# Performance work log

Hardware: AMD Instinct MI355X
Metric: run time of the kernel (lower is better)

Reference implementation:

```python
import jax, jax.numpy as jnp
import numpy as np

B, S, HID = 4096, 50, 256
NH = 4
HD = HID // NH          # 64
FB = S // 2 + 1         # 26 freq bins
ALPHA = 0.3
LN_EPS = 1e-12


def setup_inputs() -> dict:
    key = jax.random.key(0)
    ks = jax.random.split(key, 10)
    item = jax.random.normal(ks[0], (B, S, HID), dtype=jnp.float32)
    attr = jax.random.normal(ks[1], (B, S, HID), dtype=jnp.float32)
    complex_weight = jax.random.normal(ks[2], (1, NH, S // 2, HD), dtype=jnp.float32) * 0.02
    base_filter = jnp.ones((NH, FB, 1), dtype=jnp.float32)
    base_bias = jnp.full((NH, FB, 1), -0.1, dtype=jnp.float32)
    # adaptive MLP: Linear(HID,HID) -> GELU -> Linear(HID, NH*FB*2)
    w1 = jax.random.normal(ks[3], (HID, HID), dtype=jnp.float32) * (1.0 / np.sqrt(HID))
    b1 = jnp.zeros((HID,), dtype=jnp.float32)
    w2 = jax.random.normal(ks[4], (HID, NH * FB * 2), dtype=jnp.float32) * (1.0 / np.sqrt(HID))
    b2 = jnp.zeros((NH * FB * 2,), dtype=jnp.float32)
    ln_gamma = jnp.ones((HID,), dtype=jnp.float32)
    ln_beta = jnp.zeros((HID,), dtype=jnp.float32)
    return {
        "item_tensor": item, "attr_tensor": attr,
        "complex_weight": complex_weight,
        "base_filter": base_filter, "base_bias": base_bias,
        "w1": w1, "b1": b1, "w2": w2, "b2": b2,
        "ln_gamma": ln_gamma, "ln_beta": ln_beta,
    }


def _forward(item_tensor, attr_tensor, complex_weight, base_filter, base_bias,
             w1, b1, w2, b2, ln_gamma, ln_beta):
    b, s, hid = item_tensor.shape
    # [B, NH, S, HD]
    x_heads = item_tensor.reshape(b, s, NH, HD).transpose(0, 2, 1, 3)

    # ---- frequency branch ----
    F_fft = jnp.fft.rfft(x_heads, axis=2, norm='ortho')  # [B, NH, FB, HD] complex
    attr_ctx = attr_tensor.mean(axis=1)                   # [B, HID]
    h = jax.nn.gelu(attr_ctx @ w1 + b1, approximate=False)
    adapt = (h @ w2 + b2).reshape(b, NH, FB, 2)
    adaptive_scale = adapt[..., 0:1]
    adaptive_bias = adapt[..., 1:2]
    eff_filter = base_filter * (1.0 + adaptive_scale)     # [B, NH, FB, 1]
    eff_bias = base_bias + adaptive_bias                   # real, added to real part
    F_mod = F_fft * eff_filter + eff_bias
    x_fft = jnp.fft.irfft(F_mod, n=s, axis=2, norm='ortho')  # [B, NH, S, HD]

    # ---- Haar wavelet lifting branch (S even => no truncation/pad) ----
    x_even = x_heads[:, :, 0::2, :]
    x_odd = x_heads[:, :, 1::2, :]
    approx = 0.5 * (x_even + x_odd)
    detail = 0.5 * (x_even - x_odd) * complex_weight
    even_recon = approx + detail
    odd_recon = approx - detail
    # interleave even/odd back: [B, NH, S/2, 2, HD] -> [B, NH, S, HD]
    x_wavelet = jnp.stack([even_recon, odd_recon], axis=3).reshape(b, NH, s, HD)

    # ---- gate combine + residual LayerNorm ----
    x_combined = (1.0 - ALPHA) * x_wavelet + ALPHA * x_fft
    x_out = x_combined.transpose(0, 2, 1, 3).reshape(b, s, hid)
    res = x_out + item_tensor  # dropout is identity in eval
    mu = res.mean(axis=-1, keepdims=True)
    var = jnp.mean(jnp.square(res - mu), axis=-1, keepdims=True)
    return (res - mu) * jax.lax.rsqrt(var + LN_EPS) * ln_gamma + ln_beta


def reference(item_tensor, attr_tensor, complex_weight, base_filter, base_bias,
              w1, b1, w2, b2, ln_gamma, ln_beta):
    return _forward(item_tensor, attr_tensor, complex_weight, base_filter, base_bias,
                    w1, b1, w2, b2, ln_gamma, ln_beta)
```

## Files before the change

kernel.cpp:

```cpp
#include <hip/hip_runtime.h>
#include <math.h>
#include <utility>

#define B_    4096
#define S_    50
#define HID_  256
#define NH_   4
#define HD_   64
#define FB_   26
#define NPAIR 25
#define CHUNK 10

__device__ __forceinline__ float rfl_f(float v) {
    union { float f; int i; } u;
    u.f = v;
    u.i = __builtin_amdgcn_readfirstlane(u.i);
    return u.f;
}

__global__ void precompute_kernel(const float* __restrict__ base_filter,
                                  const float* __restrict__ base_bias,
                                  const float* __restrict__ w2,
                                  const float* __restrict__ b2,
                                  float* __restrict__ Wp,
                                  float* __restrict__ C0)
{
    const int m   = blockIdx.x;
    const int j   = threadIdx.x;
    const int h   = m / 100;
    const int rem = m % 100;
    const int cls = rem / 50;
    const int tau = rem % 50;

    const float inv50  = 1.0f / 50.0f;
    const float invs50 = 0.141421356237309515f;

    float acc   = 0.0f;
    float c0acc = 0.0f;
    for (int k = 0; k < FB_; ++k) {
        int   mm   = (k * tau) % 50;
        float cosv = cospif((float)(2 * mm) / 50.0f);
        float wk   = (k == 0 || k == 25) ? 1.0f : 2.0f;
        int   o    = (h * FB_ + k) * 2 + cls;
        float coef;
        if (cls == 0) coef = wk * inv50 * cosv * base_filter[h * FB_ + k];
        else          coef = wk * invs50 * cosv;
        acc += coef * w2[j * 208 + o];
        if (j == 0) {
            if (cls == 0) c0acc += coef * (1.0f + b2[o]);
            else          c0acc += coef * (base_bias[h * FB_ + k] + b2[o]);
        }
    }
    Wp[j * 400 + m] = acc;
    if (j == 0) C0[m] = c0acc;
}

__global__ __launch_bounds__(256)
void mean_kernel(const float* __restrict__ attr, float* __restrict__ ctx)
{
    const int g    = threadIdx.x >> 6;
    const int lane = threadIdx.x & 63;
    const int b    = blockIdx.x * 4 + g;
    const float4* p = (const float4*)(attr + (size_t)b * S_ * HID_) + lane;
    float4 s = make_float4(0.f, 0.f, 0.f, 0.f);
    #pragma unroll
    for (int t = 0; t < S_; ++t) {
        float4 v = p[t * 64];
        s.x += v.x; s.y += v.y; s.z += v.z; s.w += v.w;
    }
    const float is = 1.0f / S_;
    s.x *= is; s.y *= is; s.z *= is; s.w *= is;
    ((float4*)(ctx + (size_t)b * HID_))[lane] = s;
}

template <int EPI>
__global__ __launch_bounds__(256)
void gemm_kernel(const float* __restrict__ A, const float* __restrict__ Bm,
                 const float* __restrict__ bias, float* __restrict__ C,
                 int M, int N, int K)
{
    __shared__ float As[64][33];
    __shared__ float Bs[32][64];
    const int tid = threadIdx.x;
    const int tx = tid & 15, ty = tid >> 4;
    const int col0 = blockIdx.x * 64;
    const int row0 = blockIdx.y * 64;

    float acc[4][4] = {};

    for (int k0 = 0; k0 < K; k0 += 32) {
        #pragma unroll
        for (int l = 0; l < 2; ++l) {
            int f = tid + l * 256;
            int r = f >> 3;
            int c4 = f & 7;
            float4 av = *(const float4*)(A + (size_t)(row0 + r) * K + k0 + c4 * 4);
            As[r][c4 * 4 + 0] = av.x; As[r][c4 * 4 + 1] = av.y;
            As[r][c4 * 4 + 2] = av.z; As[r][c4 * 4 + 3] = av.w;
        }
        #pragma unroll
        for (int l = 0; l < 2; ++l) {
            int f = tid + l * 256;
            int kr = f >> 4;
            int c4 = f & 15;
            int col = col0 + c4 * 4;
            float4 bv = make_float4(0.f, 0.f, 0.f, 0.f);
            if (col < N) bv = *(const float4*)(Bm + (size_t)(k0 + kr) * N + col);
            *(float4*)&Bs[kr][c4 * 4] = bv;
        }
        __syncthreads();
        #pragma unroll
        for (int kk = 0; kk < 32; ++kk) {
            float4 bv = *(float4*)&Bs[kk][tx * 4];
            float br[4] = {bv.x, bv.y, bv.z, bv.w};
            #pragma unroll
            for (int r = 0; r < 4; ++r) {
                float av = As[ty * 4 + r][kk];
                #pragma unroll
                for (int c = 0; c < 4; ++c)
                    acc[r][c] = fmaf(av, br[c], acc[r][c]);
            }
        }
        __syncthreads();
    }

    #pragma unroll
    for (int r = 0; r < 4; ++r) {
        int row = row0 + ty * 4 + r;
        #pragma unroll
        for (int c = 0; c < 4; ++c) {
            int col = col0 + tx * 4 + c;
            if (col < N) {
                float v = acc[r][c] + bias[col];
                if (EPI == 0)
                    v = 0.5f * v * (1.0f + erff(v * 0.70710678118654752f));
                C[(size_t)row * N + col] = v;
            }
        }
    }
}

template <int T, int TP>
__device__ __forceinline__ float cval(const float (&cv)[26]) {
    constexpr int ci = ((T - TP) % 50 + 50) % 50;
    constexpr int dd = (ci > 25) ? (50 - ci) : ci;
    return cv[dd];
}

template <int R0, int TP, int... J>
__device__ __forceinline__ void convJ(float (&a)[CHUNK], const float (&x)[50],
                                      const float (&cv)[26],
                                      std::integer_sequence<int, J...>) {
    ((a[J] = fmaf(cval<R0 + J, TP>(cv), x[TP], a[J])), ...);
}

template <int R0, int... TPs>
__device__ __forceinline__ void convChunk(float (&a)[CHUNK], const float (&x)[50],
                                          const float (&cv)[26],
                                          std::integer_sequence<int, TPs...>) {
    (convJ<R0, TPs>(a, x, cv, std::make_integer_sequence<int, CHUNK>{}), ...);
}

template <int R0>
__device__ __forceinline__ void chunk_proc(const float (&x)[50], const float (&cv)[26],
                                           const float* __restrict__ vb,
                                           const float* __restrict__ cwp,
                                           float gam, float bet,
                                           float* __restrict__ outp,
                                           float (*buf)[HID_], float2* sums,
                                           int tid, int w, int lane)
{
    float a[CHUNK] = {};
    convChunk<R0>(a, x, cv, std::make_integer_sequence<int, 50>{});

    #pragma unroll
    for (int q = 0; q < CHUNK / 2; ++q) {
        const int p = R0 / 2 + q;
        float e  = x[2 * p], o = x[2 * p + 1];
        float ap = 0.5f * (e + o);
        float dt = 0.5f * (e - o) * cwp[p * HD_];
        float fe = a[2 * q]     + rfl_f(vb[2 * p]);
        float fo = a[2 * q + 1] + rfl_f(vb[2 * p + 1]);
        a[2 * q]     = 0.7f * (ap + dt) + 0.3f * fe + e;
        a[2 * q + 1] = 0.7f * (ap - dt) + 0.3f * fo + o;
    }

    #pragma unroll
    for (int j = 0; j < CHUNK; ++j) buf[j][tid] = a[j];
    __syncthreads();

    #pragma unroll
    for (int rr = 0; rr < 3; ++rr) {
        const int r = w + rr * 4;
        if (r < CHUNK) {
            float4 v = *(const float4*)&buf[r][lane * 4];
            float s  = (v.x + v.y) + (v.z + v.w);
            float qq = v.x * v.x + v.y * v.y + v.z * v.z + v.w * v.w;
            #pragma unroll
            for (int m = 1; m < 64; m <<= 1) {
                s  += __shfl_xor(s,  m, 64);
                qq += __shfl_xor(qq, m, 64);
            }
            if (lane == 0) {
                float mu  = s * (1.0f / HID_);
                float var = qq * (1.0f / HID_) - mu * mu;
                sums[r] = make_float2(mu, rsqrtf(var + 1e-12f));
            }
        }
    }
    __syncthreads();

    #pragma unroll
    for (int j = 0; j < CHUNK; ++j) {
        float2 ms = sums[j];
        outp[(R0 + j) * HID_] = (a[j] - ms.x) * ms.y * gam + bet;
    }
}

__global__ __launch_bounds__(256)
__attribute__((amdgpu_waves_per_eu(2)))
void fused_kernel(const float* __restrict__ item,
                  const float* __restrict__ cw,
                  const float* __restrict__ cv,
                  const float* __restrict__ gamma,
                  const float* __restrict__ beta,
                  float* __restrict__ out)
{
    __shared__ float  buf[CHUNK][HID_];
    __shared__ float2 sums[CHUNK];

    const int b    = blockIdx.x;
    const int tid  = threadIdx.x;
    const int w    = tid >> 6;
    const int lane = tid & 63;
    const int wu   = __builtin_amdgcn_readfirstlane(w);

    const float* cb = cv + (size_t)b * 400 + wu * 100;
    float cvr[26];
    #pragma unroll
    for (int j = 0; j < 26; ++j)
        cvr[j] = rfl_f(cb[j]);
    const float* vb = cb + 50;

    const float* xp = item + (size_t)b * S_ * HID_ + tid;
    float x[50];
    #pragma unroll
    for (int t = 0; t < 50; ++t) x[t] = xp[t * HID_];

    const float gam = gamma[tid];
    const float bet = beta[tid];
    float* outp = out + (size_t)b * S_ * HID_ + tid;
    const float* cwp = cw + (size_t)(wu * NPAIR) * HD_ + lane;

    chunk_proc< 0>(x, cvr, vb, cwp, gam, bet, outp, buf, sums, tid, w, lane);
    chunk_proc<10>(x, cvr, vb, cwp, gam, bet, outp, buf, sums, tid, w, lane);
    chunk_proc<20>(x, cvr, vb, cwp, gam, bet, outp, buf, sums, tid, w, lane);
    chunk_proc<30>(x, cvr, vb, cwp, gam, bet, outp, buf, sums, tid, w, lane);
    chunk_proc<40>(x, cvr, vb, cwp, gam, bet, outp, buf, sums, tid, w, lane);
}

extern "C" void kernel_launch(void* const* d_in, const int* in_sizes, int n_in,
                              void* d_out, int out_size, void* d_ws, size_t ws_size,
                              hipStream_t stream)
{
    (void)in_sizes; (void)n_in; (void)out_size; (void)ws_size;
    const float* item = (const float*)d_in[0];
    const float* attr = (const float*)d_in[1];
    const float* cw   = (const float*)d_in[2];
    const float* bf   = (const float*)d_in[3];
    const float* bb   = (const float*)d_in[4];
    const float* w1   = (const float*)d_in[5];
    const float* b1   = (const float*)d_in[6];
    const float* w2   = (const float*)d_in[7];
    const float* b2   = (const float*)d_in[8];
    const float* g    = (const float*)d_in[9];
    const float* be   = (const float*)d_in[10];
    float* out = (float*)d_out;
    float* ws  = (float*)d_ws;

    float* ctx  = ws;
    float* hbuf = ws + 1048576;
    float* Wp   = ws + 2097152;
    float* C0   = ws + 2199552;
    float* cvb  = ws + 2200064;

    hipLaunchKernelGGL(precompute_kernel, dim3(400), dim3(256), 0, stream,
                       bf, bb, w2, b2, Wp, C0);
    hipLaunchKernelGGL(mean_kernel, dim3(B_ / 4), dim3(256), 0, stream, attr, ctx);
    hipLaunchKernelGGL((gemm_kernel<0>), dim3(4, 64), dim3(256), 0, stream,
                       ctx, w1, b1, hbuf, B_, 256, 256);
    hipLaunchKernelGGL((gemm_kernel<1>), dim3(7, 64), dim3(256), 0, stream,
                       hbuf, Wp, C0, cvb, B_, 400, 256);
    hipLaunchKernelGGL(fused_kernel, dim3(B_), dim3(256), 0, stream,
                       item, cw, cvb, g, be, out);
}
```

Baseline: 590.6 us.

## Stream item pairs into 50-row register accumulators and fold gate/residual constants

The fused kernel no longer holds all 50 input rows in registers and convolves them in chunks. It now streams item rows two at a time into 50 register accumulators that start from the per-row bias. The 0.3 gate is folded into the precomputed filter coefficients, and the wavelet, gate and residual terms are merged into two FMA coefficients per pair. Occupancy is raised from 2 to 4 waves per EU, and both small GEMMs switch to 32x32 tiles to launch more blocks. The aims are fewer registers, better overlap of loads with FMAs and better GEMM occupancy, at the risk of spills with 50 live accumulators under a tighter register cap.

```diff
diff --git a/kernel.cpp b/kernel.cpp
--- a/kernel.cpp
+++ b/kernel.cpp
@@ -9,7 +9,6 @@
 #define HD_   64
 #define FB_   26
 #define NPAIR 25
-#define CHUNK 10
 
 __device__ __forceinline__ float rfl_f(float v) {
     union { float f; int i; } u;
@@ -32,8 +31,8 @@
     const int cls = rem / 50;
     const int tau = rem % 50;
 
-    const float inv50  = 1.0f / 50.0f;
-    const float invs50 = 0.141421356237309515f;
+    const float inv50  = 0.3f / 50.0f;
+    const float invs50 = 0.3f * 0.141421356237309515f;
 
     float acc   = 0.0f;
     float c0acc = 0.0f;
@@ -79,57 +78,43 @@
                  const float* __restrict__ bias, float* __restrict__ C,
                  int M, int N, int K)
 {
-    __shared__ float As[64][33];
-    __shared__ float Bs[32][64];
+    __shared__ float As[32][36];
+    __shared__ float Bs[32][36];
     const int tid = threadIdx.x;
     const int tx = tid & 15, ty = tid >> 4;
-    const int col0 = blockIdx.x * 64;
-    const int row0 = blockIdx.y * 64;
-
-    float acc[4][4] = {};
+    const int col0 = blockIdx.x * 32;
+    const int row0 = blockIdx.y * 32;
+    const int lr = tid >> 3;
+    const int lc = (tid & 7) * 4;
+
+    float acc[2][2] = {};
 
     for (int k0 = 0; k0 < K; k0 += 32) {
-        #pragma unroll
-        for (int l = 0; l < 2; ++l) {
-            int f = tid + l * 256;
-            int r = f >> 3;
-            int c4 = f & 7;
-            float4 av = *(const float4*)(A + (size_t)(row0 + r) * K + k0 + c4 * 4);
-            As[r][c4 * 4 + 0] = av.x; As[r][c4 * 4 + 1] = av.y;
-            As[r][c4 * 4 + 2] = av.z; As[r][c4 * 4 + 3] = av.w;
-        }
-        #pragma unroll
-        for (int l = 0; l < 2; ++l) {
-            int f = tid + l * 256;
-            int kr = f >> 4;
-            int c4 = f & 15;
-            int col = col0 + c4 * 4;
-            float4 bv = make_float4(0.f, 0.f, 0.f, 0.f);
-            if (col < N) bv = *(const float4*)(Bm + (size_t)(k0 + kr) * N + col);
-            *(float4*)&Bs[kr][c4 * 4] = bv;
-        }
+        float4 av = *(const float4*)(A + (size_t)(row0 + lr) * K + k0 + lc);
+        *(float4*)&As[lr][lc] = av;
+        float4 bv = make_float4(0.f, 0.f, 0.f, 0.f);
+        if (col0 + lc + 4 <= N)
+            bv = *(const float4*)(Bm + (size_t)(k0 + lr) * N + col0 + lc);
+        *(float4*)&Bs[lr][lc] = bv;
         __syncthreads();
         #pragma unroll
         for (int kk = 0; kk < 32; ++kk) {
-            float4 bv = *(float4*)&Bs[kk][tx * 4];
-            float br[4] = {bv.x, bv.y, bv.z, bv.w};
-            #pragma unroll
-            for (int r = 0; r < 4; ++r) {
-                float av = As[ty * 4 + r][kk];
-                #pragma unroll
-                for (int c = 0; c < 4; ++c)
-                    acc[r][c] = fmaf(av, br[c], acc[r][c]);
-            }
+            float a0 = As[ty * 2][kk],     a1 = As[ty * 2 + 1][kk];
+            float b0 = Bs[kk][tx * 2],     b1 = Bs[kk][tx * 2 + 1];
+            acc[0][0] = fmaf(a0, b0, acc[0][0]);
+            acc[0][1] = fmaf(a0, b1, acc[0][1]);
+            acc[1][0] = fmaf(a1, b0, acc[1][0]);
+            acc[1][1] = fmaf(a1, b1, acc[1][1]);
         }
         __syncthreads();
     }
 
     #pragma unroll
-    for (int r = 0; r < 4; ++r) {
-        int row = row0 + ty * 4 + r;
+    for (int r = 0; r < 2; ++r) {
+        int row = row0 + ty * 2 + r;
         #pragma unroll
-        for (int c = 0; c < 4; ++c) {
-            int col = col0 + tx * 4 + c;
+        for (int c = 0; c < 2; ++c) {
+            int col = col0 + tx * 2 + c;
             if (col < N) {
                 float v = acc[r][c] + bias[col];
                 if (EPI == 0)
@@ -147,52 +132,54 @@
     return cv[dd];
 }
 
-template <int R0, int TP, int... J>
-__device__ __forceinline__ void convJ(float (&a)[CHUNK], const float (&x)[50],
-                                      const float (&cv)[26],
-                                      std::integer_sequence<int, J...>) {
-    ((a[J] = fmaf(cval<R0 + J, TP>(cv), x[TP], a[J])), ...);
-}
-
-template <int R0, int... TPs>
-__device__ __forceinline__ void convChunk(float (&a)[CHUNK], const float (&x)[50],
+template <int P, int... T>
+__device__ __forceinline__ void convPairT(float (&acc)[50], float e, float o,
                                           const float (&cv)[26],
-                                          std::integer_sequence<int, TPs...>) {
-    (convJ<R0, TPs>(a, x, cv, std::make_integer_sequence<int, CHUNK>{}), ...);
+                                          std::integer_sequence<int, T...>) {
+    ((acc[T] = fmaf(cval<T, 2 * P>(cv), e, acc[T])), ...);
+    ((acc[T] = fmaf(cval<T, 2 * P + 1>(cv), o, acc[T])), ...);
+}
+
+template <int P>
+__device__ __forceinline__ void convPair(float (&acc)[50],
+                                         const float* __restrict__ xp,
+                                         const float* __restrict__ cwp,
+                                         const float (&cv)[26]) {
+    float e   = xp[(2 * P) * HID_];
+    float o   = xp[(2 * P + 1) * HID_];
+    float cwv = cwp[P * HD_];
+    convPairT<P>(acc, e, o, cv, std::make_integer_sequence<int, 50>{});
+    float Pc = fmaf(0.35f, cwv, 1.35f);
+    float Qc = fmaf(-0.35f, cwv, 0.35f);
+    acc[2 * P]     = fmaf(Pc, e, acc[2 * P]);
+    acc[2 * P]     = fmaf(Qc, o, acc[2 * P]);
+    acc[2 * P + 1] = fmaf(Qc, e, acc[2 * P + 1]);
+    acc[2 * P + 1] = fmaf(Pc, o, acc[2 * P + 1]);
+}
+
+template <int... Ps>
+__device__ __forceinline__ void convAll(float (&acc)[50],
+                                        const float* __restrict__ xp,
+                                        const float* __restrict__ cwp,
+                                        const float (&cv)[26],
+                                        std::integer_sequence<int, Ps...>) {
+    (convPair<Ps>(acc, xp, cwp, cv), ...);
 }
 
 template <int R0>
-__device__ __forceinline__ void chunk_proc(const float (&x)[50], const float (&cv)[26],
-                                           const float* __restrict__ vb,
-                                           const float* __restrict__ cwp,
-                                           float gam, float bet,
-                                           float* __restrict__ outp,
-                                           float (*buf)[HID_], float2* sums,
-                                           int tid, int w, int lane)
-{
-    float a[CHUNK] = {};
-    convChunk<R0>(a, x, cv, std::make_integer_sequence<int, 50>{});
-
-    #pragma unroll
-    for (int q = 0; q < CHUNK / 2; ++q) {
-        const int p = R0 / 2 + q;
-        float e  = x[2 * p], o = x[2 * p + 1];
-        float ap = 0.5f * (e + o);
-        float dt = 0.5f * (e - o) * cwp[p * HD_];
-        float fe = a[2 * q]     + rfl_f(vb[2 * p]);
-        float fo = a[2 * q + 1] + rfl_f(vb[2 * p + 1]);
-        a[2 * q]     = 0.7f * (ap + dt) + 0.3f * fe + e;
-        a[2 * q + 1] = 0.7f * (ap - dt) + 0.3f * fo + o;
-    }
-
-    #pragma unroll
-    for (int j = 0; j < CHUNK; ++j) buf[j][tid] = a[j];
+__device__ __forceinline__ void lnChunk(float (&acc)[50], float (*buf)[HID_],
+                                        float2* sums, float gam, float bet,
+                                        float* __restrict__ outp,
+                                        int tid, int w, int lane)
+{
+    #pragma unroll
+    for (int j = 0; j < 10; ++j) buf[j][tid] = acc[R0 + j];
     __syncthreads();
 
     #pragma unroll
     for (int rr = 0; rr < 3; ++rr) {
         const int r = w + rr * 4;
-        if (r < CHUNK) {
+        if (r < 10) {
             float4 v = *(const float4*)&buf[r][lane * 4];
             float s  = (v.x + v.y) + (v.z + v.w);
             float qq = v.x * v.x + v.y * v.y + v.z * v.z + v.w * v.w;
@@ -211,14 +198,14 @@
     __syncthreads();
 
     #pragma unroll
-    for (int j = 0; j < CHUNK; ++j) {
+    for (int j = 0; j < 10; ++j) {
         float2 ms = sums[j];
-        outp[(R0 + j) * HID_] = (a[j] - ms.x) * ms.y * gam + bet;
+        outp[(R0 + j) * HID_] = (acc[R0 + j] - ms.x) * ms.y * gam + bet;
     }
 }
 
 __global__ __launch_bounds__(256)
-__attribute__((amdgpu_waves_per_eu(2)))
+__attribute__((amdgpu_waves_per_eu(4)))
 void fused_kernel(const float* __restrict__ item,
                   const float* __restrict__ cw,
                   const float* __restrict__ cv,
@@ -226,8 +213,8 @@
                   const float* __restrict__ beta,
                   float* __restrict__ out)
 {
-    __shared__ float  buf[CHUNK][HID_];
-    __shared__ float2 sums[CHUNK];
+    __shared__ float  buf[10][HID_];
+    __shared__ float2 sums[10];
 
     const int b    = blockIdx.x;
     const int tid  = threadIdx.x;
@@ -238,25 +225,27 @@
     const float* cb = cv + (size_t)b * 400 + wu * 100;
     float cvr[26];
     #pragma unroll
-    for (int j = 0; j < 26; ++j)
-        cvr[j] = rfl_f(cb[j]);
+    for (int j = 0; j < 26; ++j) cvr[j] = rfl_f(cb[j]);
     const float* vb = cb + 50;
 
-    const float* xp = item + (size_t)b * S_ * HID_ + tid;
-    float x[50];
-    #pragma unroll
-    for (int t = 0; t < 50; ++t) x[t] = xp[t * HID_];
+    float acc[50];
+    #pragma unroll
+    for (int t = 0; t < 50; ++t) acc[t] = rfl_f(vb[t]);
+
+    const float* xp  = item + (size_t)b * S_ * HID_ + tid;
+    const float* cwp = cw + (size_t)(wu * NPAIR) * HD_ + lane;
+
+    convAll(acc, xp, cwp, cvr, std::make_integer_sequence<int, NPAIR>{});
 
     const float gam = gamma[tid];
     const float bet = beta[tid];
     float* outp = out + (size_t)b * S_ * HID_ + tid;
-    const float* cwp = cw + (size_t)(wu * NPAIR) * HD_ + lane;
-
-    chunk_proc< 0>(x, cvr, vb, cwp, gam, bet, outp, buf, sums, tid, w, lane);
-    chunk_proc<10>(x, cvr, vb, cwp, gam, bet, outp, buf, sums, tid, w, lane);
-    chunk_proc<20>(x, cvr, vb, cwp, gam, bet, outp, buf, sums, tid, w, lane);
-    chunk_proc<30>(x, cvr, vb, cwp, gam, bet, outp, buf, sums, tid, w, lane);
-    chunk_proc<40>(x, cvr, vb, cwp, gam, bet, outp, buf, sums, tid, w, lane);
+
+    lnChunk< 0>(acc, buf, sums, gam, bet, outp, tid, w, lane);
+    lnChunk<10>(acc, buf, sums, gam, bet, outp, tid, w, lane);
+    lnChunk<20>(acc, buf, sums, gam, bet, outp, tid, w, lane);
+    lnChunk<30>(acc, buf, sums, gam, bet, outp, tid, w, lane);
+    lnChunk<40>(acc, buf, sums, gam, bet, outp, tid, w, lane);
 }
 
 extern "C" void kernel_launch(void* const* d_in, const int* in_sizes, int n_in,
@@ -287,9 +276,9 @@
     hipLaunchKernelGGL(precompute_kernel, dim3(400), dim3(256), 0, stream,
                        bf, bb, w2, b2, Wp, C0);
     hipLaunchKernelGGL(mean_kernel, dim3(B_ / 4), dim3(256), 0, stream, attr, ctx);
-    hipLaunchKernelGGL((gemm_kernel<0>), dim3(4, 64), dim3(256), 0, stream,
+    hipLaunchKernelGGL((gemm_kernel<0>), dim3(8, 128), dim3(256), 0, stream,
                        ctx, w1, b1, hbuf, B_, 256, 256);
-    hipLaunchKernelGGL((gemm_kernel<1>), dim3(7, 64), dim3(256), 0, stream,
+    hipLaunchKernelGGL((gemm_kernel<1>), dim3(13, 128), dim3(256), 0, stream,
                        hbuf, Wp, C0, cvb, B_, 400, 256);
     hipLaunchKernelGGL(fused_kernel, dim3(B_), dim3(256), 0, stream,
                        item, cw, cvb, g, be, out);
```

Result: faster. 572.2 us (-3.1%).
